# Performance work log

Measured on AMD Instinct MI355X. Metric: run time of the kernel, lower is better.

## Reference

```python
import jax, jax.numpy as jnp
import numpy as np

N_OBJ, N_REL = 2048, 32768
OBJ_DIM, POOL, H, E, C = 4096, 2048, 512, 200, 151
GEO = 128
IMG_W, IMG_H = 1024.0, 768.0
NUM_ITER = 3


def _lin(x, W, b):
    return x @ W.T + b


def _gru(x, h, Wih, Whh, bih, bhh):
    # torch.nn.GRUCell math; gates stacked (r, z, n)
    gi = x @ Wih.T + bih
    gh = h @ Whh.T + bhh
    i_r, i_z, i_n = jnp.split(gi, 3, axis=-1)
    h_r, h_z, h_n = jnp.split(gh, 3, axis=-1)
    r = jax.nn.sigmoid(i_r + h_r)
    z = jax.nn.sigmoid(i_z + h_z)
    n = jnp.tanh(i_n + r * h_n)
    return (1.0 - z) * n + z * h


def _box_info(boxes, norm=None):
    # [x1,y1,x2,y2,cx,cy,w,h]
    wh = boxes[:, 2:4] - boxes[:, 0:2] + 1.0
    ctr = boxes[:, 0:2] + 0.5 * wh
    info = jnp.concatenate([boxes, ctr, wh], axis=1)
    return info / norm if norm is not None else info


def _box_pair_info(b1, b2):
    # b1,b2: [R,8] normalized box infos -> [R,32]
    ub = jnp.stack([jnp.minimum(b1[:, 0], b2[:, 0]), jnp.minimum(b1[:, 1], b2[:, 1]),
                    jnp.maximum(b1[:, 2], b2[:, 2]), jnp.maximum(b1[:, 3], b2[:, 3])], axis=1)
    ib = jnp.stack([jnp.maximum(b1[:, 0], b2[:, 0]), jnp.maximum(b1[:, 1], b2[:, 1]),
                    jnp.minimum(b1[:, 2], b2[:, 2]), jnp.minimum(b1[:, 3], b2[:, 3])], axis=1)
    inter = _box_info(ib)
    bad = (ib[:, 2] < ib[:, 0]) | (ib[:, 3] < ib[:, 1])
    inter = jnp.where(bad[:, None], 0.0, inter)
    return jnp.concatenate([b1, b2, _box_info(ub), inter], axis=1)


def _encode_box_info(boxes):
    # motifs 9-d geometry encoding
    wh = boxes[:, 2:4] - boxes[:, 0:2] + 1.0
    xy = boxes[:, 0:2] + 0.5 * wh
    w, h = wh[:, 0:1], wh[:, 1:2]
    x, y = xy[:, 0:1], xy[:, 1:2]
    x1, y1, x2, y2 = boxes[:, 0:1], boxes[:, 1:2], boxes[:, 2:3], boxes[:, 3:4]
    return jnp.concatenate([w / IMG_W, h / IMG_H, x / IMG_W, y / IMG_H, x1 / IMG_W,
                            y1 / IMG_H, x2 / IMG_W, y2 / IMG_H, w * h / (IMG_W * IMG_H)], axis=1)


def _forward(inst_roi_feats, union_features, boxes, emb_dist_W, emb_label_W, up_W, up_b,
             pairup_W, pairup_b, pos1_W, pos1_b, bn_g, bn_b, bn_m, bn_v, pos2_W, pos2_b,
             spt1_W, spt1_b, spt2_W, spt2_b, pairfin_W, pairfin_b, objhid_W, objhid_b,
             objfin_W, objfin_b, objU_W, objU_b, edgeU_W, edgeU_b,
             egru_Wih, egru_Whh, egru_bih, egru_bhh, ngru_Wih, ngru_Whh, ngru_bih, ngru_bhh,
             svw_W, svw_b, ovw_W, ovw_b, obj_labels, sub_idx, obj_idx):
    # ---- PairwiseFeatureExtractor ----
    # pos_embed: fc(9,32) -> eval BatchNorm1d(32) -> fc(32,128) -> ReLU
    p = _lin(_encode_box_info(boxes), pos1_W, pos1_b)
    p = (p - bn_m) * bn_g / jnp.sqrt(bn_v + 1e-5) + bn_b
    pos_embed = jax.nn.relu(_lin(p, pos2_W, pos2_b))
    emb_dist = emb_dist_W[obj_labels]                       # predcls: embed GT labels
    aug = _lin(jnp.concatenate([inst_roi_feats, emb_dist, pos_embed], 1), objhid_W, objhid_b)
    augment = jnp.concatenate([emb_label_W[obj_labels], inst_roi_feats, aug], 1)  # [N,4808]
    # pairwise (edge) features: gather head/tail reps + spatial gating
    obox = _box_info(boxes, norm=max(IMG_W, IMG_H, 100.0))  # [N,8]
    fused = _lin(augment, pairup_W, pairup_b).reshape(-1, 2, H)
    pair = jnp.concatenate([fused[:, 0][sub_idx], fused[:, 1][obj_idx]], 1)  # [R,1024]
    geo = _box_pair_info(obox[sub_idx], obox[obj_idx])      # [R,32]
    spt = jax.nn.relu(_lin(jax.nn.relu(_lin(geo, spt1_W, spt1_b)), spt2_W, spt2_b))
    rel_feats = jax.nn.relu(_lin(pair * spt, pairfin_W, pairfin_b))
    rel_feats = rel_feats + _lin(union_features, up_W, up_b)  # 'fusion' + dim-up
    obj_feats = jax.nn.relu(_lin(augment, objfin_W, objfin_b))
    # ---- IMP iterative message passing ----
    obj_rep = _lin(obj_feats, objU_W, objU_b)
    rel_rep = jax.nn.relu(_lin(rel_feats, edgeU_W, edgeU_b))
    vert = _gru(obj_rep, jnp.zeros_like(obj_rep), ngru_Wih, ngru_Whh, ngru_bih, ngru_bhh)
    edge = _gru(rel_rep, jnp.zeros_like(rel_rep), egru_Wih, egru_Whh, egru_bih, egru_bhh)
    n = vert.shape[0]
    for _ in range(NUM_ITER):
        sv, ov = vert[sub_idx], vert[obj_idx]
        ws = jax.nn.sigmoid(_lin(jnp.concatenate([sv, edge], 1), svw_W, svw_b))  # [R,1]
        wo = jax.nn.sigmoid(_lin(jnp.concatenate([ov, edge], 1), ovw_W, ovw_b))
        new_edge = _gru(ws * sv + wo * ov, edge, egru_Wih, egru_Whh, egru_bih, egru_bhh)
        # sub2rel @ (ws*edge) + obj2rel @ (wo*edge) == segment sums over pair indices
        ctx = jax.ops.segment_sum(ws * edge, sub_idx, n) + jax.ops.segment_sum(wo * edge, obj_idx, n)
        vert = _gru(ctx, vert, ngru_Wih, ngru_Whh, ngru_bih, ngru_bhh)
        edge = new_edge
    return vert, edge


def setup_inputs() -> dict:
    keys = jax.random.split(jax.random.key(0), 64)
    ki = iter(keys)

    def nrm(shape, s=0.02):
        return (jax.random.normal(next(ki), shape) * s).astype(jnp.float32)

    kb = jax.random.split(next(ki), 4)
    x1 = jax.random.uniform(kb[0], (N_OBJ,)) * (IMG_W - 200.0)
    y1 = jax.random.uniform(kb[1], (N_OBJ,)) * (IMG_H - 150.0)
    x2 = x1 + 1.0 + jax.random.uniform(kb[2], (N_OBJ,)) * 199.0
    y2 = y1 + 1.0 + jax.random.uniform(kb[3], (N_OBJ,)) * 149.0
    boxes = jnp.stack([x1, y1, x2, y2], axis=1).astype(jnp.float32)

    inp = {
        'inst_roi_feats': nrm((N_OBJ, OBJ_DIM), 1.0),
        'union_features': nrm((N_REL, OBJ_DIM), 1.0),
        'boxes': boxes,
        'emb_dist_W': nrm((C, E)), 'emb_label_W': nrm((C, E)),
        'up_W': nrm((POOL, OBJ_DIM)), 'up_b': jnp.zeros((POOL,), jnp.float32),
        'pairup_W': nrm((2 * H, H + OBJ_DIM + E)), 'pairup_b': jnp.zeros((2 * H,), jnp.float32),
        'pos1_W': nrm((32, 9)), 'pos1_b': jnp.zeros((32,), jnp.float32),
        'bn_g': jnp.ones((32,), jnp.float32), 'bn_b': jnp.zeros((32,), jnp.float32),
        'bn_m': nrm((32,)), 'bn_v': jnp.ones((32,), jnp.float32),
        'pos2_W': nrm((GEO, 32)), 'pos2_b': jnp.zeros((GEO,), jnp.float32),
        'spt1_W': nrm((H, 32)), 'spt1_b': jnp.zeros((H,), jnp.float32),
        'spt2_W': nrm((2 * H, H)), 'spt2_b': jnp.zeros((2 * H,), jnp.float32),
        'pairfin_W': nrm((POOL, 2 * H)), 'pairfin_b': jnp.zeros((POOL,), jnp.float32),
        'objhid_W': nrm((H, OBJ_DIM + E + GEO)), 'objhid_b': jnp.zeros((H,), jnp.float32),
        'objfin_W': nrm((POOL, H + OBJ_DIM + E)), 'objfin_b': jnp.zeros((POOL,), jnp.float32),
        'objU_W': nrm((H, POOL)), 'objU_b': jnp.zeros((H,), jnp.float32),
        'edgeU_W': nrm((H, POOL)), 'edgeU_b': jnp.zeros((H,), jnp.float32),
        'egru_Wih': nrm((3 * H, H)), 'egru_Whh': nrm((3 * H, H)),
        'egru_bih': jnp.zeros((3 * H,), jnp.float32), 'egru_bhh': jnp.zeros((3 * H,), jnp.float32),
        'ngru_Wih': nrm((3 * H, H)), 'ngru_Whh': nrm((3 * H, H)),
        'ngru_bih': jnp.zeros((3 * H,), jnp.float32), 'ngru_bhh': jnp.zeros((3 * H,), jnp.float32),
        'svw_W': nrm((1, 2 * H)), 'svw_b': jnp.zeros((1,), jnp.float32),
        'ovw_W': nrm((1, 2 * H)), 'ovw_b': jnp.zeros((1,), jnp.float32),
        'obj_labels': jax.random.randint(next(ki), (N_OBJ,), 0, C),
        'sub_idx': jax.random.randint(next(ki), (N_REL,), 0, N_OBJ),
        'obj_idx': jax.random.randint(next(ki), (N_REL,), 0, N_OBJ),
    }
    return inp


def reference(inst_roi_feats, union_features, boxes, emb_dist_W, emb_label_W, up_W, up_b,
              pairup_W, pairup_b, pos1_W, pos1_b, bn_g, bn_b, bn_m, bn_v, pos2_W, pos2_b,
              spt1_W, spt1_b, spt2_W, spt2_b, pairfin_W, pairfin_b, objhid_W, objhid_b,
              objfin_W, objfin_b, objU_W, objU_b, edgeU_W, edgeU_b,
              egru_Wih, egru_Whh, egru_bih, egru_bhh, ngru_Wih, ngru_Whh, ngru_bih, ngru_bhh,
              svw_W, svw_b, ovw_W, ovw_b, obj_labels, sub_idx, obj_idx):
    return _forward(inst_roi_feats, union_features, boxes, emb_dist_W, emb_label_W, up_W, up_b,
                    pairup_W, pairup_b, pos1_W, pos1_b, bn_g, bn_b, bn_m, bn_v, pos2_W, pos2_b,
                    spt1_W, spt1_b, spt2_W, spt2_b, pairfin_W, pairfin_b, objhid_W, objhid_b,
                    objfin_W, objfin_b, objU_W, objU_b, edgeU_W, edgeU_b,
                    egru_Wih, egru_Whh, egru_bih, egru_bhh, ngru_Wih, ngru_Whh, ngru_bih, ngru_bhh,
                    svw_W, svw_b, ovw_W, ovw_b, obj_labels, sub_idx, obj_idx)
```

## Files before the change

### kernel.cpp

```cpp
#include <hip/hip_runtime.h>
#include <stdint.h>

#define NOBJ 2048
#define NREL 32768

typedef __attribute__((ext_vector_type(8))) short short8;
typedef __attribute__((ext_vector_type(4))) float f32x4;
typedef __attribute__((ext_vector_type(4))) unsigned short ushort4v;

__device__ __forceinline__ unsigned short f2bs(float x){
  unsigned u = __float_as_uint(x);
  unsigned v = u + 0x7fffu + ((u >> 16) & 1u);
  return (unsigned short)(v >> 16);
}
__device__ __forceinline__ float b2f(unsigned short u){
  return __uint_as_float(((unsigned)u) << 16);
}
__device__ __forceinline__ float sigf(float x){ return 1.0f / (1.0f + expf(-x)); }

__device__ __forceinline__ void gload16(const unsigned short* g, unsigned short* l) {
  __builtin_amdgcn_global_load_lds(
      (const __attribute__((address_space(1))) unsigned int*)(uintptr_t)g,
      (__attribute__((address_space(3))) unsigned int*)(uintptr_t)l,
      16, 0, 0);
}

template<int RMODE, bool ACCUM, bool OUTB, bool PRODF, bool AF32>
__global__ __launch_bounds__(256, 2)
void gemm_bt(const void* __restrict__ Ap, const unsigned short* __restrict__ B,
             const float* __restrict__ bias, const float* __restrict__ Cin,
             void* __restrict__ Cp, int M, int N, int K, int lda, int ldc,
             const unsigned short* __restrict__ fusedp,
             const int* __restrict__ subp, const int* __restrict__ objp)
{
  __shared__ __align__(16) unsigned short As[128 * 64];
  __shared__ __align__(16) unsigned short Bs[128 * 64];
  const int t = threadIdx.x;
  const int lane = t & 63;
  const int w = t >> 6;
  const int nwg = gridDim.x;
  const int q8 = nwg >> 3, r8 = nwg & 7;
  const int xcd = blockIdx.x & 7, bidx = blockIdx.x >> 3;
  const int wgid = (xcd < r8 ? xcd * (q8 + 1) : r8 * (q8 + 1) + (xcd - r8) * q8) + bidx;
  const int ntile = N >> 7;
  const int bm = wgid / ntile;
  const int bn = wgid - bm * ntile;
  const int m0 = bm << 7, n0 = bn << 7;
  const int wm = (w & 1) << 6, wn = (w >> 1) << 6;
  const int lrow = lane & 15, kg = lane >> 4;
  const int rx = lrow & 7;

  const int srow8 = lane >> 3;
  const int sslot = ((lane & 7) ^ srow8) << 3;
  const unsigned short* Bg = B + (long)(n0 + w * 8 + srow8) * K + sslot;
  const long ldb32 = (long)32 * K;

  const unsigned short* Ag = nullptr;
  const float* afp = nullptr;
  long lda32 = 0;
  int ar0 = 0;
  unsigned short* abase = nullptr;
  if constexpr (AF32) {
    ar0 = t >> 4;
    const int ac4 = t & 15;
    afp = (const float*)Ap + (long)(m0 + ar0) * lda + (ac4 << 2);
    abase = As + ((((ac4 >> 1) ^ (ar0 & 7)) << 3) + ((ac4 & 1) << 2));
  } else {
    Ag = (const unsigned short*)Ap + (long)(m0 + w * 8 + srow8) * lda + sslot;
    lda32 = (long)32 * lda;
  }

  f32x4 acc[4][4] = {};

  for (int k0 = 0; k0 < K; k0 += 64) {
#pragma unroll
    for (int q = 0; q < 4; q++)
      gload16(Bg + q * ldb32 + k0, Bs + (q * 32 + w * 8) * 64);
    if constexpr (AF32) {
      const float* ap = afp + k0;
#pragma unroll
      for (int j = 0; j < 8; j++) {
        f32x4 v = *(const f32x4*)(ap + (long)j * 16 * lda);
        ushort4v o;
        o[0] = f2bs(v[0]); o[1] = f2bs(v[1]); o[2] = f2bs(v[2]); o[3] = f2bs(v[3]);
        *(ushort4v*)(abase + (ar0 + j * 16) * 64) = o;
      }
    } else {
#pragma unroll
      for (int q = 0; q < 4; q++)
        gload16(Ag + q * lda32 + k0, As + (q * 32 + w * 8) * 64);
    }
    __syncthreads();
    short8 afr[4][2], bfr[4][2];
#pragma unroll
    for (int i = 0; i < 4; i++) {
      const int ra = wm + i * 16 + lrow;
#pragma unroll
      for (int ks = 0; ks < 2; ks++)
        afr[i][ks] = *(const short8*)(As + ra * 64 + (((ks * 4 + kg) ^ rx) << 3));
    }
#pragma unroll
    for (int j = 0; j < 4; j++) {
      const int rb = wn + j * 16 + lrow;
#pragma unroll
      for (int ks = 0; ks < 2; ks++)
        bfr[j][ks] = *(const short8*)(Bs + rb * 64 + (((ks * 4 + kg) ^ rx) << 3));
    }
#pragma unroll
    for (int i = 0; i < 4; i++)
#pragma unroll
      for (int j = 0; j < 4; j++)
#pragma unroll
        for (int ks = 0; ks < 2; ks++)
          acc[i][j] = __builtin_amdgcn_mfma_f32_16x16x32_bf16(afr[i][ks], bfr[j][ks], acc[i][j], 0, 0, 0);
    __syncthreads();
  }

  float* Cf = (float*)Cp;
  unsigned short* Cb = (unsigned short*)Cp;
#pragma unroll
  for (int i = 0; i < 4; i++) {
#pragma unroll
    for (int j = 0; j < 4; j++) {
      const int col = n0 + wn + j * 16 + lrow;
      const float bv = bias[col];
#pragma unroll
      for (int q = 0; q < 4; q++) {
        const long row = m0 + wm + i * 16 + kg * 4 + q;
        float v = acc[i][j][q] + bv;
        if constexpr (RMODE == 1) v = fmaxf(v, 0.0f);
        if constexpr (PRODF) {
          int gr = (col < 512) ? subp[row] : objp[row];
          v *= b2f(fusedp[(long)gr * 1024 + col]);
        }
        if constexpr (ACCUM) v += Cin[row * (long)N + col];
        if constexpr (RMODE == 2) v = fmaxf(v, 0.0f);
        if constexpr (OUTB) Cb[row * (long)ldc + col] = f2bs(v);
        else Cf[row * (long)ldc + col] = v;
      }
    }
  }
}

template<int RMODE>
__global__ __launch_bounds__(256, 2)
void gemm64(const unsigned short* __restrict__ A, const unsigned short* __restrict__ B,
            const float* __restrict__ bias, unsigned short* __restrict__ C,
            int M, int N, int K, int lda, int ldc)
{
  __shared__ __align__(16) unsigned short As[64 * 64];
  __shared__ __align__(16) unsigned short Bs[64 * 64];
  const int t = threadIdx.x;
  const int lane = t & 63;
  const int w = t >> 6;
  const int nwg = gridDim.x;
  const int q8 = nwg >> 3, r8 = nwg & 7;
  const int xcd = blockIdx.x & 7, bidx = blockIdx.x >> 3;
  const int wgid = (xcd < r8 ? xcd * (q8 + 1) : r8 * (q8 + 1) + (xcd - r8) * q8) + bidx;
  const int ntile = N >> 6;
  const int bm = wgid / ntile, bn = wgid - bm * ntile;
  const int m0 = bm << 6, n0 = bn << 6;
  const int wm = (w & 1) << 5, wn = (w >> 1) << 5;
  const int lrow = lane & 15, kg = lane >> 4;
  const int rx = lrow & 7;

  const int srow8 = lane >> 3;
  const int sslot = ((lane & 7) ^ srow8) << 3;
  const unsigned short* Ag = A + (long)(m0 + w * 16 + srow8) * lda + sslot;
  const unsigned short* Bg = B + (long)(n0 + w * 16 + srow8) * K + sslot;
  const long lda8 = 8L * lda, ldb8 = 8L * K;

  f32x4 acc[2][2] = {};

  for (int k0 = 0; k0 < K; k0 += 64) {
    gload16(Ag + k0,        As + (w * 16) * 64);
    gload16(Ag + lda8 + k0, As + (w * 16 + 8) * 64);
    gload16(Bg + k0,        Bs + (w * 16) * 64);
    gload16(Bg + ldb8 + k0, Bs + (w * 16 + 8) * 64);
    __syncthreads();
    short8 afr[2][2], bfr[2][2];
#pragma unroll
    for (int i = 0; i < 2; i++) {
      const int ra = wm + i * 16 + lrow;
#pragma unroll
      for (int ks = 0; ks < 2; ks++)
        afr[i][ks] = *(const short8*)(As + ra * 64 + (((ks * 4 + kg) ^ rx) << 3));
    }
#pragma unroll
    for (int j = 0; j < 2; j++) {
      const int rb = wn + j * 16 + lrow;
#pragma unroll
      for (int ks = 0; ks < 2; ks++)
        bfr[j][ks] = *(const short8*)(Bs + rb * 64 + (((ks * 4 + kg) ^ rx) << 3));
    }
#pragma unroll
    for (int i = 0; i < 2; i++)
#pragma unroll
      for (int j = 0; j < 2; j++)
#pragma unroll
        for (int ks = 0; ks < 2; ks++)
          acc[i][j] = __builtin_amdgcn_mfma_f32_16x16x32_bf16(afr[i][ks], bfr[j][ks], acc[i][j], 0, 0, 0);
    __syncthreads();
  }

#pragma unroll
  for (int i = 0; i < 2; i++) {
#pragma unroll
    for (int j = 0; j < 2; j++) {
      const int col = n0 + wn + j * 16 + lrow;
      const float bv = bias[col];
#pragma unroll
      for (int q = 0; q < 4; q++) {
        const long row = m0 + wm + i * 16 + kg * 4 + q;
        float v = acc[i][j][q] + bv;
        if constexpr (RMODE == 1) v = fmaxf(v, 0.0f);
        C[row * (long)ldc + col] = f2bs(v);
      }
    }
  }
}


__global__ void cvt_pad4(const float* __restrict__ src, unsigned short* __restrict__ dst,
                         int rows, int K0, int Kp)
{
  const int kp4 = Kp >> 2;
  const long total = (long)rows * kp4;
  for (long i = blockIdx.x * (long)blockDim.x + threadIdx.x; i < total; i += (long)gridDim.x * blockDim.x) {
    int r = (int)(i / kp4), k = (int)(i - (long)r * kp4) << 2;
    ushort4v o;
    if (k < K0) {
      f32x4 v = *(const f32x4*)(src + (long)r * K0 + k);
      o[0] = f2bs(v[0]); o[1] = f2bs(v[1]); o[2] = f2bs(v[2]); o[3] = f2bs(v[3]);
    } else {
      o[0] = 0; o[1] = 0; o[2] = 0; o[3] = 0;
    }
    *(ushort4v*)(dst + (long)r * Kp + k) = o;
  }
}

struct CvtSeg { const float* src; unsigned short* dst; long base; long n4; };
struct Cvt9 { CvtSeg s[9]; long total; };

__global__ void cvt4_multi(Cvt9 cfg)
{
  for (long i = blockIdx.x * (long)blockDim.x + threadIdx.x; i < cfg.total;
       i += (long)gridDim.x * blockDim.x) {
#pragma unroll
    for (int k = 0; k < 9; k++) {
      if (i >= cfg.s[k].base && i < cfg.s[k].base + cfg.s[k].n4) {
        long j = i - cfg.s[k].base;
        f32x4 v = ((const f32x4*)cfg.s[k].src)[j];
        ushort4v o;
        o[0] = f2bs(v[0]); o[1] = f2bs(v[1]); o[2] = f2bs(v[2]); o[3] = f2bs(v[3]);
        ((ushort4v*)cfg.s[k].dst)[j] = o;
        break;
      }
    }
  }
}

__global__ void transpose_cvt(const float* __restrict__ src, unsigned short* __restrict__ dst,
                              int R, int C)
{
  __shared__ float tile[32][33];
  int c0 = blockIdx.x * 32, r0 = blockIdx.y * 32;
  for (int i = threadIdx.y; i < 32; i += 8)
    tile[i][threadIdx.x] = src[(long)(r0 + i) * C + c0 + threadIdx.x];
  __syncthreads();
  for (int i = threadIdx.y; i < 32; i += 8)
    dst[(long)(c0 + i) * R + r0 + threadIdx.x] = f2bs(tile[threadIdx.x][i]);
}

__global__ void comp_bias(const float* __restrict__ edgeU_W, const float* __restrict__ up_b,
                          const float* __restrict__ edgeU_b, float* __restrict__ b_comp)
{
  int j = (int)((blockIdx.x * (long)blockDim.x + threadIdx.x) >> 6);
  int l = threadIdx.x & 63;
  if (j >= 512) return;
  float s = 0.0f;
  for (int k = l; k < 2048; k += 64) s += edgeU_W[(long)j * 2048 + k] * up_b[k];
#pragma unroll
  for (int off = 32; off > 0; off >>= 1) s += __shfl_xor(s, off);
  if (l == 0) b_comp[j] = s + edgeU_b[j];
}

__global__ void bias_cat(const float* __restrict__ bhh, float* __restrict__ out)
{
  int j = blockIdx.x * blockDim.x + threadIdx.x;
  if (j < 3072) out[j] = (j < 1536) ? 0.0f : bhh[j - 1536];
}

__global__ void obox_k(const float* __restrict__ boxes, float* __restrict__ obox)
{
  int i = blockIdx.x * blockDim.x + threadIdx.x;
  if (i >= NOBJ) return;
  float x1 = boxes[i*4], y1 = boxes[i*4+1], x2 = boxes[i*4+2], y2 = boxes[i*4+3];
  float wdt = x2 - x1 + 1.0f, hgt = y2 - y1 + 1.0f;
  float cx = x1 + 0.5f * wdt, cy = y1 + 0.5f * hgt;
  const float inv = 1.0f / 1024.0f;
  float* o = obox + i * 8;
  o[0]=x1*inv; o[1]=y1*inv; o[2]=x2*inv; o[3]=y2*inv;
  o[4]=cx*inv; o[5]=cy*inv; o[6]=wdt*inv; o[7]=hgt*inv;
}

__global__ void posembed_k(const float* __restrict__ boxes,
                           const float* __restrict__ w1, const float* __restrict__ b1,
                           const float* __restrict__ g, const float* __restrict__ bb,
                           const float* __restrict__ mm, const float* __restrict__ vv,
                           const float* __restrict__ w2, const float* __restrict__ b2,
                           float* __restrict__ out)
{
  int o = blockIdx.x, t = threadIdx.x;
  __shared__ float e[9];
  __shared__ float p[32];
  if (t == 0) {
    float x1 = boxes[o*4], y1 = boxes[o*4+1], x2 = boxes[o*4+2], y2 = boxes[o*4+3];
    float wdt = x2 - x1 + 1.0f, hgt = y2 - y1 + 1.0f;
    float cx = x1 + 0.5f * wdt, cy = y1 + 0.5f * hgt;
    e[0]=wdt/1024.0f; e[1]=hgt/768.0f; e[2]=cx/1024.0f; e[3]=cy/768.0f;
    e[4]=x1/1024.0f;  e[5]=y1/768.0f;  e[6]=x2/1024.0f; e[7]=y2/768.0f;
    e[8]=wdt*hgt/(1024.0f*768.0f);
  }
  __syncthreads();
  if (t < 32) {
    float s = b1[t];
#pragma unroll
    for (int j = 0; j < 9; j++) s += w1[t*9+j] * e[j];
    s = (s - mm[t]) * g[t] / sqrtf(vv[t] + 1e-5f) + bb[t];
    p[t] = s;
  }
  __syncthreads();
  float s = b2[t];
#pragma unroll
  for (int j = 0; j < 32; j++) s += w2[t*32+j] * p[j];
  out[o*128 + t] = fmaxf(s, 0.0f);
}

__device__ __forceinline__ void pack8_store(unsigned short* dst, f32x4 a, f32x4 b)
{
  ushort4v o0, o1;
  o0[0]=f2bs(a[0]); o0[1]=f2bs(a[1]); o0[2]=f2bs(a[2]); o0[3]=f2bs(a[3]);
  o1[0]=f2bs(b[0]); o1[1]=f2bs(b[1]); o1[2]=f2bs(b[2]); o1[3]=f2bs(b[3]);
  *(ushort4v*)dst = o0;
  *(ushort4v*)(dst + 4) = o1;
}

__global__ void build_x1(const float* __restrict__ inst, const float* __restrict__ embd,
                         const int* __restrict__ labels, const float* __restrict__ pose,
                         unsigned short* __restrict__ X1b)
{
  const long total = (long)NOBJ * 560;
  for (long i = blockIdx.x * (long)blockDim.x + threadIdx.x; i < total; i += (long)gridDim.x * blockDim.x) {
    int r = (int)(i / 560), c = ((int)(i - (long)r * 560)) << 3;
    unsigned short* dst = X1b + (long)r * 4480 + c;
    const float* src;
    if (c < 4096)      src = inst + (long)r * 4096 + c;
    else if (c < 4296) src = embd + (long)labels[r] * 200 + (c - 4096);
    else if (c < 4424) src = pose + r * 128 + (c - 4296);
    else { ushort4v z = {0,0,0,0}; *(ushort4v*)dst = z; *(ushort4v*)(dst+4) = z; continue; }
    pack8_store(dst, *(const f32x4*)src, *((const f32x4*)src + 1));
  }
}

__global__ void build_aug(const float* __restrict__ embl, const int* __restrict__ labels,
                          const float* __restrict__ inst, unsigned short* __restrict__ augb)
{
  const long total = (long)NOBJ * 608;
  for (long i = blockIdx.x * (long)blockDim.x + threadIdx.x; i < total; i += (long)gridDim.x * blockDim.x) {
    int r = (int)(i / 608), c = ((int)(i - (long)r * 608)) << 3;
    if (c >= 4296 && c < 4808) continue;
    unsigned short* dst = augb + (long)r * 4864 + c;
    const float* src;
    if (c < 200)       src = embl + (long)labels[r] * 200 + c;
    else if (c < 4296) src = inst + (long)r * 4096 + (c - 200);
    else { ushort4v z = {0,0,0,0}; *(ushort4v*)dst = z; *(ushort4v*)(dst+4) = z; continue; }
    pack8_store(dst, *(const f32x4*)src, *((const f32x4*)src + 1));
  }
}

__global__ void build_geo(const float* __restrict__ obox, const int* __restrict__ sub,
                          const int* __restrict__ obj, unsigned short* __restrict__ geob)
{
  int r = blockIdx.x * blockDim.x + threadIdx.x;
  if (r >= NREL) return;
  const float* b1 = obox + sub[r] * 8;
  const float* b2 = obox + obj[r] * 8;
  float o[32];
#pragma unroll
  for (int j = 0; j < 8; j++) { o[j] = b1[j]; o[8+j] = b2[j]; }
  float ux1 = fminf(b1[0], b2[0]), uy1 = fminf(b1[1], b2[1]);
  float ux2 = fmaxf(b1[2], b2[2]), uy2 = fmaxf(b1[3], b2[3]);
  float uw = ux2 - ux1 + 1.0f, uh = uy2 - uy1 + 1.0f;
  o[16]=ux1; o[17]=uy1; o[18]=ux2; o[19]=uy2;
  o[20]=ux1+0.5f*uw; o[21]=uy1+0.5f*uh; o[22]=uw; o[23]=uh;
  float ix1 = fmaxf(b1[0], b2[0]), iy1 = fmaxf(b1[1], b2[1]);
  float ix2 = fminf(b1[2], b2[2]), iy2 = fminf(b1[3], b2[3]);
  bool bad = (ix2 < ix1) || (iy2 < iy1);
  float iw = ix2 - ix1 + 1.0f, ih = iy2 - iy1 + 1.0f;
  if (bad) {
#pragma unroll
    for (int j = 24; j < 32; j++) o[j] = 0.0f;
  } else {
    o[24]=ix1; o[25]=iy1; o[26]=ix2; o[27]=iy2;
    o[28]=ix1+0.5f*iw; o[29]=iy1+0.5f*ih; o[30]=iw; o[31]=ih;
  }
  unsigned short* gp = geob + (long)r * 64;
#pragma unroll
  for (int j = 0; j < 32; j++) gp[j] = f2bs(o[j]);
#pragma unroll
  for (int j = 32; j < 64; j++) gp[j] = 0;
}

__global__ void gru_init_v(const unsigned short* __restrict__ gi, const float* __restrict__ bhh,
                           float* __restrict__ h, unsigned short* __restrict__ hb, int n)
{
  const long total = (long)n * 64;
  for (long i = blockIdx.x * (long)blockDim.x + threadIdx.x; i < total; i += (long)gridDim.x * blockDim.x) {
    int r = (int)(i >> 6), c = ((int)(i & 63)) << 3;
    const unsigned short* gr = gi + (long)r * 1536;
    short8 vr = *(const short8*)(gr + c);
    short8 vz = *(const short8*)(gr + 512 + c);
    short8 vn = *(const short8*)(gr + 1024 + c);
    float hv[8];
#pragma unroll
    for (int k = 0; k < 8; k++) {
      float rr = sigf(b2f((unsigned short)vr[k]) + bhh[c + k]);
      float z  = sigf(b2f((unsigned short)vz[k]) + bhh[512 + c + k]);
      float nn = tanhf(b2f((unsigned short)vn[k]) + rr * bhh[1024 + c + k]);
      hv[k] = (1.0f - z) * nn;
    }
    float* hp = h + (long)r * 512 + c;
    *(f32x4*)hp = *(f32x4*)hv;
    *(f32x4*)(hp + 4) = *(f32x4*)(hv + 4);
    pack8_store(hb + (long)r * 512 + c, *(f32x4*)hv, *(f32x4*)(hv + 4));
  }
}

__global__ void gru_init_e(const unsigned short* __restrict__ gi, const float* __restrict__ bhh,
                           unsigned short* __restrict__ hb, int n)
{
  const long total = (long)n * 64;
  for (long i = blockIdx.x * (long)blockDim.x + threadIdx.x; i < total; i += (long)gridDim.x * blockDim.x) {
    int r = (int)(i >> 6), c = ((int)(i & 63)) << 3;
    const unsigned short* gr = gi + (long)r * 1536;
    short8 vr = *(const short8*)(gr + c);
    short8 vz = *(const short8*)(gr + 512 + c);
    short8 vn = *(const short8*)(gr + 1024 + c);
    float hv[8];
#pragma unroll
    for (int k = 0; k < 8; k++) {
      float rr = sigf(b2f((unsigned short)vr[k]) + bhh[c + k]);
      float z  = sigf(b2f((unsigned short)vz[k]) + bhh[512 + c + k]);
      float nn = tanhf(b2f((unsigned short)vn[k]) + rr * bhh[1024 + c + k]);
      hv[k] = (1.0f - z) * nn;
    }
    pack8_store(hb + (long)r * 512 + c, *(f32x4*)hv, *(f32x4*)(hv + 4));
  }
}

__global__ void gru_step_v(const unsigned short* __restrict__ gi, const unsigned short* __restrict__ gh,
                           int ghs, const float* __restrict__ hin, float* __restrict__ hout,
                           unsigned short* __restrict__ hb, int n)
{
  const long total = (long)n * 64;
  for (long i = blockIdx.x * (long)blockDim.x + threadIdx.x; i < total; i += (long)gridDim.x * blockDim.x) {
    int r = (int)(i >> 6), c = ((int)(i & 63)) << 3;
    const unsigned short* gr = gi + (long)r * 1536;
    const unsigned short* hr = gh + (long)r * ghs;
    short8 ir = *(const short8*)(gr + c);
    short8 iz = *(const short8*)(gr + 512 + c);
    short8 in_ = *(const short8*)(gr + 1024 + c);
    short8 hrr = *(const short8*)(hr + c);
    short8 hz = *(const short8*)(hr + 512 + c);
    short8 hn = *(const short8*)(hr + 1024 + c);
    const float* hi = hin + (long)r * 512 + c;
    f32x4 h0 = *(const f32x4*)hi;
    f32x4 h1 = *(const f32x4*)(hi + 4);
    float hv[8];
#pragma unroll
    for (int k = 0; k < 8; k++) {
      float rr = sigf(b2f((unsigned short)ir[k]) + b2f((unsigned short)hrr[k]));
      float z  = sigf(b2f((unsigned short)iz[k]) + b2f((unsigned short)hz[k]));
      float nn = tanhf(b2f((unsigned short)in_[k]) + rr * b2f((unsigned short)hn[k]));
      float old = (k < 4) ? h0[k] : h1[k - 4];
      hv[k] = (1.0f - z) * nn + z * old;
    }
    float* hp = hout + (long)r * 512 + c;
    *(f32x4*)hp = *(f32x4*)hv;
    *(f32x4*)(hp + 4) = *(f32x4*)(hv + 4);
    pack8_store(hb + (long)r * 512 + c, *(f32x4*)hv, *(f32x4*)(hv + 4));
  }
}

__global__ __launch_bounds__(256)
void gru_step_e2(const unsigned short* __restrict__ GH, const unsigned short* __restrict__ VG,
                 const float* __restrict__ ws_arr_in, const float* __restrict__ wo_arr_in,
                 float* __restrict__ ws_arr_out, float* __restrict__ wo_arr_out,
                 const int* __restrict__ sub, const int* __restrict__ obj,
                 const float* __restrict__ bih,
                 unsigned short* __restrict__ edgeb, float* __restrict__ fout,
                 const unsigned short* __restrict__ vertb,
                 const float* __restrict__ svwW, const float* __restrict__ svwb,
                 const float* __restrict__ ovwW, const float* __restrict__ ovwb,
                 int compute_w, int n)
{
  long gid = blockIdx.x * 256L + threadIdx.x;
  int r = (int)(gid >> 6);
  int l = (int)(gid & 63);
  if (r >= n) return;
  const int c = l << 3;
  int s = sub[r], o = obj[r];
  float ws = ws_arr_in[r], wo = wo_arr_in[r];
  const unsigned short* gh = GH + (long)r * 1536;
  const unsigned short* vs = VG + (long)s * 3072;
  const unsigned short* vo = VG + (long)o * 3072;
  short8 ghr = *(const short8*)(gh + c);
  short8 ghz = *(const short8*)(gh + 512 + c);
  short8 ghn = *(const short8*)(gh + 1024 + c);
  short8 vsr = *(const short8*)(vs + c);
  short8 vsz = *(const short8*)(vs + 512 + c);
  short8 vsn = *(const short8*)(vs + 1024 + c);
  short8 vor_ = *(const short8*)(vo + c);
  short8 voz = *(const short8*)(vo + 512 + c);
  short8 von = *(const short8*)(vo + 1024 + c);
  short8 hold = *(const short8*)(edgeb + (long)r * 512 + c);
  float hv[8];
#pragma unroll
  for (int k = 0; k < 8; k++) {
    float gir = ws * b2f((unsigned short)vsr[k]) + wo * b2f((unsigned short)vor_[k]) + bih[c + k];
    float giz = ws * b2f((unsigned short)vsz[k]) + wo * b2f((unsigned short)voz[k]) + bih[512 + c + k];
    float gin = ws * b2f((unsigned short)vsn[k]) + wo * b2f((unsigned short)von[k]) + bih[1024 + c + k];
    float rr = sigf(gir + b2f((unsigned short)ghr[k]));
    float z  = sigf(giz + b2f((unsigned short)ghz[k]));
    float nn = tanhf(gin + rr * b2f((unsigned short)ghn[k]));
    hv[k] = (1.0f - z) * nn + z * b2f((unsigned short)hold[k]);
  }
  pack8_store(edgeb + (long)r * 512 + c, *(f32x4*)hv, *(f32x4*)(hv + 4));
  if (fout) {
    float* fp = fout + (long)r * 512 + c;
    *(f32x4*)fp = *(f32x4*)hv;
    *(f32x4*)(fp + 4) = *(f32x4*)(hv + 4);
  }
  if (compute_w) {
    short8 svv = *(const short8*)(vertb + (long)s * 512 + c);
    short8 ovv = *(const short8*)(vertb + (long)o * 512 + c);
    float as = 0.0f, ao = 0.0f;
#pragma unroll
    for (int k = 0; k < 8; k++) {
      float e = hv[k];
      as += svwW[c + k] * b2f((unsigned short)svv[k]) + svwW[512 + c + k] * e;
      ao += ovwW[c + k] * b2f((unsigned short)ovv[k]) + ovwW[512 + c + k] * e;
    }
#pragma unroll
    for (int off = 32; off > 0; off >>= 1) {
      as += __shfl_xor(as, off);
      ao += __shfl_xor(ao, off);
    }
    if (l == 0) {
      ws_arr_out[r] = sigf(as + svwb[0]);
      wo_arr_out[r] = sigf(ao + ovwb[0]);
    }
  }
}

__global__ __launch_bounds__(256)
void edge_weights(const unsigned short* __restrict__ vertb, const unsigned short* __restrict__ edgeb,
                  const int* __restrict__ sub, const int* __restrict__ obj,
                  const float* __restrict__ svwW, const float* __restrict__ svwb,
                  const float* __restrict__ ovwW, const float* __restrict__ ovwb,
                  float* __restrict__ ws_arr, float* __restrict__ wo_arr)
{
  long gid = blockIdx.x * 256L + threadIdx.x;
  int r = (int)(gid >> 6);
  int l = (int)(gid & 63);
  if (r >= NREL) return;
  int s = sub[r], o = obj[r];
  const unsigned short* sv = vertb + (long)s * 512;
  const unsigned short* ov = vertb + (long)o * 512;
  const unsigned short* e  = edgeb + (long)r * 512;
  float as = 0.0f, ao = 0.0f;
#pragma unroll
  for (int k = 0; k < 8; k++) {
    int c = l + k * 64;
    float svv = b2f(sv[c]), ovv = b2f(ov[c]), ev = b2f(e[c]);
    as += svwW[c] * svv + svwW[512 + c] * ev;
    ao += ovwW[c] * ovv + ovwW[512 + c] * ev;
  }
#pragma unroll
  for (int off = 32; off > 0; off >>= 1) {
    as += __shfl_xor(as, off);
    ao += __shfl_xor(ao, off);
  }
  if (l == 0) {
    ws_arr[r] = sigf(as + svwb[0]);
    wo_arr[r] = sigf(ao + ovwb[0]);
  }
}


__global__ void csr_count(const int* __restrict__ sub, const int* __restrict__ obj,
                          int* __restrict__ cnt)
{
  int r = blockIdx.x * blockDim.x + threadIdx.x;
  if (r >= NREL) return;
  atomicAdd(&cnt[sub[r]], 1);
  atomicAdd(&cnt[obj[r]], 1);
}

__global__ __launch_bounds__(1024)
void csr_scan(const int* __restrict__ cnt, int* __restrict__ off)
{
  __shared__ int a[1024], b[1024];
  int t = threadIdx.x;
  int c0 = cnt[2*t], c1 = cnt[2*t+1];
  a[t] = c0 + c1;
  __syncthreads();
  int* src = a; int* dst = b;
  for (int s = 1; s < 1024; s <<= 1) {
    int v = src[t];
    if (t >= s) v += src[t - s];
    dst[t] = v;
    __syncthreads();
    int* tmp = src; src = dst; dst = tmp;
  }
  int incl = src[t];
  int excl = incl - (c0 + c1);
  off[2*t] = excl;
  off[2*t+1] = excl + c0;
  if (t == 1023) off[2048] = incl;
}

__global__ void csr_fill(const int* __restrict__ sub, const int* __restrict__ obj,
                         const int* __restrict__ off, int* __restrict__ rcur,
                         int* __restrict__ lists)
{
  int r = blockIdx.x * blockDim.x + threadIdx.x;
  if (r >= NREL) return;
  int s = sub[r];
  int p = atomicAdd(&rcur[s], 1);
  lists[off[s] + p] = (r << 1);
  int o = obj[r];
  int q = atomicAdd(&rcur[o], 1);
  lists[off[o] + q] = (r << 1) | 1;
}

__global__ __launch_bounds__(128)
void ctx_gather(const unsigned short* __restrict__ edgeb, const float* __restrict__ ws,
                const float* __restrict__ wo, const int* __restrict__ off,
                const int* __restrict__ lists, unsigned short* __restrict__ ctxb)
{
  __shared__ float part[512];
  int o = blockIdx.x;
  int l = threadIdx.x & 63;
  int w = threadIdx.x >> 6;
  int i0 = off[o], i1 = off[o + 1];
  float acc[8] = {0.f,0.f,0.f,0.f,0.f,0.f,0.f,0.f};
  for (int i = i0 + w; i < i1; i += 2) {
    int e = lists[i];
    int r = e >> 1;
    float sc = (e & 1) ? wo[r] : ws[r];
    short8 row = *(const short8*)(edgeb + (long)r * 512 + l * 8);
#pragma unroll
    for (int k = 0; k < 8; k++) acc[k] += sc * b2f((unsigned short)row[k]);
  }
  if (w == 1) {
    *(f32x4*)&part[l*8]     = *(f32x4*)&acc[0];
    *(f32x4*)&part[l*8 + 4] = *(f32x4*)&acc[4];
  }
  __syncthreads();
  if (w == 0) {
#pragma unroll
    for (int k = 0; k < 8; k++) acc[k] += part[l*8 + k];
    pack8_store(ctxb + (long)o * 512 + l * 8, *(f32x4*)&acc[0], *(f32x4*)&acc[4]);
  }
}


static inline int nblk(long total) {
  long b = (total + 255) / 256;
  return (int)(b > 16384 ? 16384 : b);
}

#define GEMM(RM, AC, OB, PF, grid, Aa, Bb, bb, Ci, Cc, Mm, Nn, Kk, ldA, ldC, fp, sp, op) \
  gemm_bt<RM, AC, OB, PF, false><<<grid, 256, 0, stream>>>(Aa, Bb, bb, Ci, Cc, Mm, Nn, Kk, ldA, ldC, fp, sp, op)
#define GEMMF(RM, AC, OB, grid, Aa, Bb, bb, Ci, Cc, Mm, Nn, Kk, ldA, ldC) \
  gemm_bt<RM, AC, OB, false, true><<<grid, 256, 0, stream>>>(Aa, Bb, bb, Ci, Cc, Mm, Nn, Kk, ldA, ldC, nullptr, nullptr, nullptr)
#define G64(RM, Aa, Bb, bb, Cc, Mm, Nn, Kk, ldA, ldC) \
  gemm64<RM><<<dim3(((Mm) >> 6) * ((Nn) >> 6)), 256, 0, stream>>>(Aa, Bb, bb, Cc, Mm, Nn, Kk, ldA, ldC)

extern "C" void kernel_launch(void* const* d_in, const int* in_sizes, int n_in,
                              void* d_out, int out_size, void* d_ws, size_t ws_size,
                              hipStream_t stream)
{
  const float* inst     = (const float*)d_in[0];
  const float* unionf   = (const float*)d_in[1];
  const float* boxes    = (const float*)d_in[2];
  const float* embd_W   = (const float*)d_in[3];
  const float* embl_W   = (const float*)d_in[4];
  const float* up_W     = (const float*)d_in[5];
  const float* up_b     = (const float*)d_in[6];
  const float* pairup_W = (const float*)d_in[7];
  const float* pairup_b = (const float*)d_in[8];
  const float* pos1_W   = (const float*)d_in[9];
  const float* pos1_b   = (const float*)d_in[10];
  const float* bn_g     = (const float*)d_in[11];
  const float* bn_b     = (const float*)d_in[12];
  const float* bn_m     = (const float*)d_in[13];
  const float* bn_v     = (const float*)d_in[14];
  const float* pos2_W   = (const float*)d_in[15];
  const float* pos2_b   = (const float*)d_in[16];
  const float* spt1_W   = (const float*)d_in[17];
  const float* spt1_b   = (const float*)d_in[18];
  const float* spt2_W   = (const float*)d_in[19];
  const float* spt2_b   = (const float*)d_in[20];
  const float* pairfin_W= (const float*)d_in[21];
  const float* pairfin_b= (const float*)d_in[22];
  const float* objhid_W = (const float*)d_in[23];
  const float* objhid_b = (const float*)d_in[24];
  const float* objfin_W = (const float*)d_in[25];
  const float* objfin_b = (const float*)d_in[26];
  const float* objU_W   = (const float*)d_in[27];
  const float* objU_b   = (const float*)d_in[28];
  const float* edgeU_W  = (const float*)d_in[29];
  const float* edgeU_b  = (const float*)d_in[30];
  const float* egru_Wih = (const float*)d_in[31];
  const float* egru_Whh = (const float*)d_in[32];
  const float* egru_bih = (const float*)d_in[33];
  const float* egru_bhh = (const float*)d_in[34];
  const float* ngru_Wih = (const float*)d_in[35];
  const float* ngru_Whh = (const float*)d_in[36];
  const float* ngru_bih = (const float*)d_in[37];
  const float* ngru_bhh = (const float*)d_in[38];
  const float* svw_W    = (const float*)d_in[39];
  const float* svw_b    = (const float*)d_in[40];
  const float* ovw_W    = (const float*)d_in[41];
  const float* ovw_b    = (const float*)d_in[42];
  const int*   labels   = (const int*)d_in[43];
  const int*   sub      = (const int*)d_in[44];
  const int*   obj      = (const int*)d_in[45];
  (void)in_sizes; (void)n_in; (void)out_size; (void)ws_size;

  char* base = (char*)d_ws;
  size_t off = 0;
  auto alloc = [&](size_t bytes) -> void* {
    void* p = base + off;
    off += (bytes + 255) & ~(size_t)255;
    return p;
  };

  unsigned short* objhid_Wb  = (unsigned short*)alloc(512L  * 4480 * 2);
  unsigned short* pairup_Wb  = (unsigned short*)alloc(1024L * 4864 * 2);
  unsigned short* objfin_Wb  = (unsigned short*)alloc(2048L * 4864 * 2);
  unsigned short* up_Wtb     = (unsigned short*)alloc(4096L * 2048 * 2);
  unsigned short* pairfin_Wb = (unsigned short*)alloc(2048L * 1024 * 2);
  unsigned short* spt1_Wb    = (unsigned short*)alloc(512L  * 64   * 2);
  unsigned short* spt2_Wb    = (unsigned short*)alloc(1024L * 512  * 2);
  unsigned short* objU_Wb    = (unsigned short*)alloc(512L  * 2048 * 2);
  unsigned short* edgeU_Wb   = (unsigned short*)alloc(512L  * 2048 * 2);
  unsigned short* egru_Wihb  = (unsigned short*)alloc(1536L * 512  * 2);
  unsigned short* egru_Whhb  = (unsigned short*)alloc(1536L * 512  * 2);
  unsigned short* ngru_Wihb  = (unsigned short*)alloc(1536L * 512  * 2);
  unsigned short* vg_Wb      = (unsigned short*)alloc(3072L * 512  * 2);
  unsigned short* W_compb    = (unsigned short*)alloc(512L  * 4096 * 2);
  float*          b_comp     = (float*)alloc(512L * 4);
  float*          zbias      = (float*)alloc(4096L * 4);
  float*          vgbias     = (float*)alloc(3072L * 4);

  float*          obox      = (float*)alloc(NOBJ * 8L * 4);
  float*          pose      = (float*)alloc(NOBJ * 128L * 4);
  unsigned short* obj_featsb= (unsigned short*)alloc((long)NOBJ * 2048 * 2);
  unsigned short* obj_repb  = (unsigned short*)alloc((long)NOBJ * 512 * 2);
  unsigned short* giv       = (unsigned short*)alloc((long)NOBJ * 1536 * 2);
  unsigned short* VGb       = (unsigned short*)alloc((long)NOBJ * 3072 * 2);
  float*          vert      = (float*)alloc((long)NOBJ * 512 * 4);
  unsigned short* vertb     = (unsigned short*)alloc((long)NOBJ * 512 * 2);
  unsigned short* ctxb      = (unsigned short*)alloc((long)NOBJ * 512 * 2);
  unsigned short* geob      = (unsigned short*)alloc((long)NREL * 64 * 2);
  unsigned short* edgeb     = (unsigned short*)alloc((long)NREL * 512 * 2);
  float*          ws_arr    = (float*)alloc((long)NREL * 4);
  float*          wo_arr    = (float*)alloc((long)NREL * 4);

  int* cnt   = (int*)alloc(NOBJ * 4);
  int* coff  = (int*)alloc((NOBJ + 1) * 4);
  int* rcur  = (int*)alloc(NOBJ * 4);
  int* lists = (int*)alloc(2L * NREL * 4);

  char* regA = (char*)alloc((long)NREL * 512 * 4);
  unsigned short* X1b = (unsigned short*)regA;
  float*          T1  = (float*)regA;
  char* regB = (char*)alloc((long)NOBJ * 4864 * 2 > (long)NREL * 512 * 2
                            ? (long)NOBJ * 4864 * 2 : (long)NREL * 512 * 2);
  unsigned short* augb     = (unsigned short*)regB;
  unsigned short* rel_repb = (unsigned short*)regB;
  unsigned short* fusedb = (unsigned short*)alloc((long)NOBJ * 1024 * 2);
  unsigned short* spt1b  = (unsigned short*)alloc((long)NREL * 512 * 2);
  char* big1 = (char*)alloc((long)NREL * 1536 * 4);
  unsigned short* G1    = (unsigned short*)big1;
  unsigned short* prodb = (unsigned short*)(big1 + (long)NREL * 1024 * 4);
  unsigned short* gi_e  = (unsigned short*)big1;
  unsigned short* GHb   = (unsigned short*)big1;

  float* d_out_vert = (float*)d_out;
  float* d_out_edge = (float*)d_out + (long)NOBJ * 512;

  cvt_pad4<<<nblk(512L*4480/4),  256, 0, stream>>>(objhid_W,  objhid_Wb,  512,  4424, 4480);
  cvt_pad4<<<nblk(1024L*4864/4), 256, 0, stream>>>(pairup_W,  pairup_Wb,  1024, 4808, 4864);
  cvt_pad4<<<nblk(2048L*4864/4), 256, 0, stream>>>(objfin_W,  objfin_Wb,  2048, 4808, 4864);
  cvt_pad4<<<nblk(512L*64/4),    256, 0, stream>>>(spt1_W,    spt1_Wb,    512,  32,   64);
  {
    Cvt9 cfg;
    long b = 0;
    auto seg = [&](int k, const float* s, unsigned short* d, long n4) {
      cfg.s[k].src = s; cfg.s[k].dst = d; cfg.s[k].base = b; cfg.s[k].n4 = n4; b += n4;
    };
    seg(0, pairfin_W, pairfin_Wb, 2048L*1024/4);
    seg(1, spt2_W,    spt2_Wb,    1024L*512/4);
    seg(2, objU_W,    objU_Wb,    512L*2048/4);
    seg(3, edgeU_W,   edgeU_Wb,   512L*2048/4);
    seg(4, egru_Wih,  egru_Wihb,  1536L*512/4);
    seg(5, egru_Whh,  egru_Whhb,  1536L*512/4);
    seg(6, ngru_Wih,  ngru_Wihb,  1536L*512/4);
    seg(7, egru_Wih,  vg_Wb,              1536L*512/4);
    seg(8, ngru_Whh,  vg_Wb + 1536L*512,  1536L*512/4);
    cfg.total = b;
    cvt4_multi<<<nblk(b), 256, 0, stream>>>(cfg);
  }
  bias_cat<<<12, 256, 0, stream>>>(ngru_bhh, vgbias);
  transpose_cvt<<<dim3(4096/32, 2048/32), dim3(32, 8), 0, stream>>>(up_W, up_Wtb, 2048, 4096);
  hipMemsetAsync(zbias, 0, 4096L * 4, stream);
  comp_bias<<<128, 256, 0, stream>>>(edgeU_W, up_b, edgeU_b, b_comp);
  G64(0, edgeU_Wb, up_Wtb, zbias, W_compb, 512, 4096, 2048, 2048, 4096);

  hipMemsetAsync(cnt, 0, NOBJ * 4, stream);
  hipMemsetAsync(rcur, 0, NOBJ * 4, stream);
  csr_count<<<NREL/256, 256, 0, stream>>>(sub, obj, cnt);
  csr_scan<<<1, 1024, 0, stream>>>(cnt, coff);
  csr_fill<<<NREL/256, 256, 0, stream>>>(sub, obj, coff, rcur, lists);

  obox_k<<<(NOBJ + 255) / 256, 256, 0, stream>>>(boxes, obox);
  posembed_k<<<NOBJ, 128, 0, stream>>>(boxes, pos1_W, pos1_b, bn_g, bn_b, bn_m, bn_v,
                                       pos2_W, pos2_b, pose);
  build_x1<<<nblk((long)NOBJ*560), 256, 0, stream>>>(inst, embd_W, labels, pose, X1b);
  build_aug<<<nblk((long)NOBJ*608), 256, 0, stream>>>(embl_W, labels, inst, augb);
  G64(0, X1b, objhid_Wb, objhid_b, augb + 4296, NOBJ, 512, 4480, 4480, 4864);
  G64(0, augb, pairup_Wb, pairup_b, fusedb, NOBJ, 1024, 4864, 4864, 1024);
  G64(1, augb, objfin_Wb, objfin_b, obj_featsb, NOBJ, 2048, 4864, 4864, 2048);
  G64(0, obj_featsb, objU_Wb, objU_b, obj_repb, NOBJ, 512, 2048, 2048, 512);
  G64(0, obj_repb, ngru_Wihb, ngru_bih, giv, NOBJ, 1536, 512, 512, 1536);
  gru_init_v<<<nblk((long)NOBJ*64), 256, 0, stream>>>(giv, ngru_bhh, vert, vertb, NOBJ);

  build_geo<<<(NREL + 255) / 256, 256, 0, stream>>>(obox, sub, obj, geob);
  GEMM(1,false,true ,false, dim3((NREL>>7)*(512>>7)),  geob, spt1_Wb, spt1_b, nullptr, spt1b, NREL, 512, 64, 64, 512, nullptr, nullptr, nullptr);
  GEMM(1,false,true ,true , dim3((NREL>>7)*(1024>>7)), spt1b, spt2_Wb, spt2_b, nullptr, prodb, NREL, 1024, 512, 512, 1024, fusedb, sub, obj);
  GEMM(1,false,true ,false, dim3((NREL>>7)*(2048>>7)), prodb, pairfin_Wb, pairfin_b, nullptr, G1, NREL, 2048, 1024, 1024, 2048, nullptr, nullptr, nullptr);
  GEMMF(0,false,false, dim3((NREL>>7)*(512>>7)), unionf, W_compb, b_comp, nullptr, T1, NREL, 512, 4096, 4096, 512);
  GEMM(2,true ,true ,false, dim3((NREL>>7)*(512>>7)),  G1, edgeU_Wb, zbias, T1, rel_repb, NREL, 512, 2048, 2048, 512, nullptr, nullptr, nullptr);
  GEMM(0,false,true ,false, dim3((NREL>>7)*(1536>>7)), rel_repb, egru_Wihb, egru_bih, nullptr, gi_e, NREL, 1536, 512, 512, 1536, nullptr, nullptr, nullptr);
  gru_init_e<<<nblk((long)NREL*64), 256, 0, stream>>>(gi_e, egru_bhh, edgeb, NREL);

  edge_weights<<<NREL*64/256, 256, 0, stream>>>(vertb, edgeb, sub, obj,
                                                svw_W, svw_b, ovw_W, ovw_b, ws_arr, wo_arr);

  for (int it = 0; it < 3; it++) {
    const bool last = (it == 2);
    ctx_gather<<<NOBJ, 128, 0, stream>>>(edgeb, ws_arr, wo_arr, coff, lists, ctxb);
    G64(0, vertb, vg_Wb, vgbias, VGb, NOBJ, 3072, 512, 512, 3072);
    GEMM(0,false,true,false, dim3((NREL>>7)*(1536>>7)), edgeb, egru_Whhb, egru_bhh, nullptr, GHb, NREL, 1536, 512, 512, 1536, nullptr, nullptr, nullptr);
    G64(0, ctxb, ngru_Wihb, ngru_bih, giv, NOBJ, 1536, 512, 512, 1536);
    gru_step_v<<<nblk((long)NOBJ*64), 256, 0, stream>>>(giv, VGb + 1536, 3072, vert,
                                                        last ? d_out_vert : vert, vertb, NOBJ);
    gru_step_e2<<<NREL*64/256, 256, 0, stream>>>(GHb, VGb, ws_arr, wo_arr, ws_arr, wo_arr,
                                                 sub, obj, egru_bih, edgeb,
                                                 last ? d_out_edge : nullptr, vertb,
                                                 svw_W, svw_b, ovw_W, ovw_b,
                                                 last ? 0 : 1, NREL);
  }
}
```

Baseline: 1.695 ms.

## Double-buffer LDS tiles in GEMM kernels and store intermediate T1 as bf16

Both GEMM kernels now use two LDS buffers and prefetch the tiles two k-steps ahead, with explicit vmcnt waits and raw barriers, so global loads overlap with MFMA work. gemm64 raises its launch_bounds occupancy hint from 2 to 4. The union-feature GEMM intermediate T1 is now written as bf16 and read back as bf16 in the accumulating GEMM, which halves that traffic at some precision cost. Doubling LDS in gemm_bt to 64KB may reduce occupancy, and the hand-written waitcnt counts must match the number of issued loads exactly.

```diff
diff --git a/kernel.cpp b/kernel.cpp
--- a/kernel.cpp
+++ b/kernel.cpp
@@ -25,16 +25,16 @@
       16, 0, 0);
 }
 
-template<int RMODE, bool ACCUM, bool OUTB, bool PRODF, bool AF32>
+template<int RMODE, bool ACCUM, bool OUTB, bool PRODF, bool AF32, bool CINB>
 __global__ __launch_bounds__(256, 2)
 void gemm_bt(const void* __restrict__ Ap, const unsigned short* __restrict__ B,
-             const float* __restrict__ bias, const float* __restrict__ Cin,
+             const float* __restrict__ bias, const void* __restrict__ Cin,
              void* __restrict__ Cp, int M, int N, int K, int lda, int ldc,
              const unsigned short* __restrict__ fusedp,
              const int* __restrict__ subp, const int* __restrict__ objp)
 {
-  __shared__ __align__(16) unsigned short As[128 * 64];
-  __shared__ __align__(16) unsigned short Bs[128 * 64];
+  __shared__ __align__(16) unsigned short As[2][128 * 64];
+  __shared__ __align__(16) unsigned short Bs[2][128 * 64];
   const int t = threadIdx.x;
   const int lane = t & 63;
   const int w = t >> 6;
@@ -58,53 +58,74 @@
   const unsigned short* Ag = nullptr;
   const float* afp = nullptr;
   long lda32 = 0;
-  int ar0 = 0;
-  unsigned short* abase = nullptr;
+  int ar0 = 0, aoff = 0;
   if constexpr (AF32) {
     ar0 = t >> 4;
     const int ac4 = t & 15;
     afp = (const float*)Ap + (long)(m0 + ar0) * lda + (ac4 << 2);
-    abase = As + ((((ac4 >> 1) ^ (ar0 & 7)) << 3) + ((ac4 & 1) << 2));
+    aoff = (((ac4 >> 1) ^ (ar0 & 7)) << 3) + ((ac4 & 1) << 2);
   } else {
     Ag = (const unsigned short*)Ap + (long)(m0 + w * 8 + srow8) * lda + sslot;
     lda32 = (long)32 * lda;
   }
 
-  f32x4 acc[4][4] = {};
-
-  for (int k0 = 0; k0 < K; k0 += 64) {
+  const int NT = K >> 6;
+
+  auto stage = [&](int buf, int kt) {
+    const unsigned short* bsrc = Bg + (long)kt * 64;
 #pragma unroll
     for (int q = 0; q < 4; q++)
-      gload16(Bg + q * ldb32 + k0, Bs + (q * 32 + w * 8) * 64);
+      gload16(bsrc + q * ldb32, Bs[buf] + (q * 32 + w * 8) * 64);
     if constexpr (AF32) {
-      const float* ap = afp + k0;
+      const float* ap = afp + (long)kt * 64;
 #pragma unroll
       for (int j = 0; j < 8; j++) {
         f32x4 v = *(const f32x4*)(ap + (long)j * 16 * lda);
         ushort4v o;
         o[0] = f2bs(v[0]); o[1] = f2bs(v[1]); o[2] = f2bs(v[2]); o[3] = f2bs(v[3]);
-        *(ushort4v*)(abase + (ar0 + j * 16) * 64) = o;
+        *(ushort4v*)(As[buf] + aoff + (ar0 + j * 16) * 64) = o;
       }
     } else {
+      const unsigned short* asrc = Ag + (long)kt * 64;
 #pragma unroll
       for (int q = 0; q < 4; q++)
-        gload16(Ag + q * lda32 + k0, As + (q * 32 + w * 8) * 64);
-    }
-    __syncthreads();
+        gload16(asrc + q * lda32, As[buf] + (q * 32 + w * 8) * 64);
+    }
+  };
+
+  f32x4 acc[4][4] = {};
+
+  stage(0, 0);
+  if (NT > 1) stage(1, 1);
+
+  for (int kt = 0; kt < NT; ++kt) {
+    const int cur = kt & 1;
+    if (kt + 1 < NT) {
+      if constexpr (AF32) asm volatile("s_waitcnt vmcnt(4)" ::: "memory");
+      else                asm volatile("s_waitcnt vmcnt(8)" ::: "memory");
+    } else {
+      asm volatile("s_waitcnt vmcnt(0)" ::: "memory");
+    }
+    asm volatile("s_waitcnt lgkmcnt(0)" ::: "memory");
+    __builtin_amdgcn_s_barrier();
+    asm volatile("" ::: "memory");
+
+    const unsigned short* As_ = As[cur];
+    const unsigned short* Bs_ = Bs[cur];
     short8 afr[4][2], bfr[4][2];
 #pragma unroll
     for (int i = 0; i < 4; i++) {
       const int ra = wm + i * 16 + lrow;
 #pragma unroll
       for (int ks = 0; ks < 2; ks++)
-        afr[i][ks] = *(const short8*)(As + ra * 64 + (((ks * 4 + kg) ^ rx) << 3));
+        afr[i][ks] = *(const short8*)(As_ + ra * 64 + (((ks * 4 + kg) ^ rx) << 3));
     }
 #pragma unroll
     for (int j = 0; j < 4; j++) {
       const int rb = wn + j * 16 + lrow;
 #pragma unroll
       for (int ks = 0; ks < 2; ks++)
-        bfr[j][ks] = *(const short8*)(Bs + rb * 64 + (((ks * 4 + kg) ^ rx) << 3));
+        bfr[j][ks] = *(const short8*)(Bs_ + rb * 64 + (((ks * 4 + kg) ^ rx) << 3));
     }
 #pragma unroll
     for (int i = 0; i < 4; i++)
@@ -113,7 +134,10 @@
 #pragma unroll
         for (int ks = 0; ks < 2; ks++)
           acc[i][j] = __builtin_amdgcn_mfma_f32_16x16x32_bf16(afr[i][ks], bfr[j][ks], acc[i][j], 0, 0, 0);
-    __syncthreads();
+    asm volatile("" ::: "memory");
+    __builtin_amdgcn_s_barrier();
+    asm volatile("" ::: "memory");
+    if (kt + 2 < NT) stage(cur, kt + 2);
   }
 
   float* Cf = (float*)Cp;
@@ -133,7 +157,10 @@
           int gr = (col < 512) ? subp[row] : objp[row];
           v *= b2f(fusedp[(long)gr * 1024 + col]);
         }
-        if constexpr (ACCUM) v += Cin[row * (long)N + col];
+        if constexpr (ACCUM) {
+          if constexpr (CINB) v += b2f(((const unsigned short*)Cin)[row * (long)N + col]);
+          else                v += ((const float*)Cin)[row * (long)N + col];
+        }
         if constexpr (RMODE == 2) v = fmaxf(v, 0.0f);
         if constexpr (OUTB) Cb[row * (long)ldc + col] = f2bs(v);
         else Cf[row * (long)ldc + col] = v;
@@ -143,13 +170,13 @@
 }
 
 template<int RMODE>
-__global__ __launch_bounds__(256, 2)
+__global__ __launch_bounds__(256, 4)
 void gemm64(const unsigned short* __restrict__ A, const unsigned short* __restrict__ B,
             const float* __restrict__ bias, unsigned short* __restrict__ C,
             int M, int N, int K, int lda, int ldc)
 {
-  __shared__ __align__(16) unsigned short As[64 * 64];
-  __shared__ __align__(16) unsigned short Bs[64 * 64];
+  __shared__ __align__(16) unsigned short As[2][64 * 64];
+  __shared__ __align__(16) unsigned short Bs[2][64 * 64];
   const int t = threadIdx.x;
   const int lane = t & 63;
   const int w = t >> 6;
@@ -169,29 +196,45 @@
   const unsigned short* Ag = A + (long)(m0 + w * 16 + srow8) * lda + sslot;
   const unsigned short* Bg = B + (long)(n0 + w * 16 + srow8) * K + sslot;
   const long lda8 = 8L * lda, ldb8 = 8L * K;
+  const int NT = K >> 6;
+
+  auto stage = [&](int buf, int kt) {
+    const unsigned short* a_ = Ag + (long)kt * 64;
+    const unsigned short* b_ = Bg + (long)kt * 64;
+    gload16(a_,        As[buf] + (w * 16) * 64);
+    gload16(a_ + lda8, As[buf] + (w * 16 + 8) * 64);
+    gload16(b_,        Bs[buf] + (w * 16) * 64);
+    gload16(b_ + ldb8, Bs[buf] + (w * 16 + 8) * 64);
+  };
 
   f32x4 acc[2][2] = {};
 
-  for (int k0 = 0; k0 < K; k0 += 64) {
-    gload16(Ag + k0,        As + (w * 16) * 64);
-    gload16(Ag + lda8 + k0, As + (w * 16 + 8) * 64);
-    gload16(Bg + k0,        Bs + (w * 16) * 64);
-    gload16(Bg + ldb8 + k0, Bs + (w * 16 + 8) * 64);
-    __syncthreads();
+  stage(0, 0);
+  if (NT > 1) stage(1, 1);
+
+  for (int kt = 0; kt < NT; ++kt) {
+    const int cur = kt & 1;
+    if (kt + 1 < NT) asm volatile("s_waitcnt vmcnt(4)" ::: "memory");
+    else             asm volatile("s_waitcnt vmcnt(0)" ::: "memory");
+    __builtin_amdgcn_s_barrier();
+    asm volatile("" ::: "memory");
+
+    const unsigned short* As_ = As[cur];
+    const unsigned short* Bs_ = Bs[cur];
     short8 afr[2][2], bfr[2][2];
 #pragma unroll
     for (int i = 0; i < 2; i++) {
       const int ra = wm + i * 16 + lrow;
 #pragma unroll
       for (int ks = 0; ks < 2; ks++)
-        afr[i][ks] = *(const short8*)(As + ra * 64 + (((ks * 4 + kg) ^ rx) << 3));
+        afr[i][ks] = *(const short8*)(As_ + ra * 64 + (((ks * 4 + kg) ^ rx) << 3));
     }
 #pragma unroll
     for (int j = 0; j < 2; j++) {
       const int rb = wn + j * 16 + lrow;
 #pragma unroll
       for (int ks = 0; ks < 2; ks++)
-        bfr[j][ks] = *(const short8*)(Bs + rb * 64 + (((ks * 4 + kg) ^ rx) << 3));
+        bfr[j][ks] = *(const short8*)(Bs_ + rb * 64 + (((ks * 4 + kg) ^ rx) << 3));
     }
 #pragma unroll
     for (int i = 0; i < 2; i++)
@@ -200,7 +243,10 @@
 #pragma unroll
         for (int ks = 0; ks < 2; ks++)
           acc[i][j] = __builtin_amdgcn_mfma_f32_16x16x32_bf16(afr[i][ks], bfr[j][ks], acc[i][j], 0, 0, 0);
-    __syncthreads();
+    asm volatile("" ::: "memory");
+    __builtin_amdgcn_s_barrier();
+    asm volatile("" ::: "memory");
+    if (kt + 2 < NT) stage(cur, kt + 2);
   }
 
 #pragma unroll
@@ -683,9 +729,11 @@
 }
 
 #define GEMM(RM, AC, OB, PF, grid, Aa, Bb, bb, Ci, Cc, Mm, Nn, Kk, ldA, ldC, fp, sp, op) \
-  gemm_bt<RM, AC, OB, PF, false><<<grid, 256, 0, stream>>>(Aa, Bb, bb, Ci, Cc, Mm, Nn, Kk, ldA, ldC, fp, sp, op)
-#define GEMMF(RM, AC, OB, grid, Aa, Bb, bb, Ci, Cc, Mm, Nn, Kk, ldA, ldC) \
-  gemm_bt<RM, AC, OB, false, true><<<grid, 256, 0, stream>>>(Aa, Bb, bb, Ci, Cc, Mm, Nn, Kk, ldA, ldC, nullptr, nullptr, nullptr)
+  gemm_bt<RM, AC, OB, PF, false, false><<<grid, 256, 0, stream>>>(Aa, Bb, bb, Ci, Cc, Mm, Nn, Kk, ldA, ldC, fp, sp, op)
+#define GEMMCB(RM, grid, Aa, Bb, bb, Ci, Cc, Mm, Nn, Kk, ldA, ldC) \
+  gemm_bt<RM, true, true, false, false, true><<<grid, 256, 0, stream>>>(Aa, Bb, bb, Ci, Cc, Mm, Nn, Kk, ldA, ldC, nullptr, nullptr, nullptr)
+#define GEMMF(RM, grid, Aa, Bb, bb, Cc, Mm, Nn, Kk, ldA, ldC) \
+  gemm_bt<RM, false, true, false, true, false><<<grid, 256, 0, stream>>>(Aa, Bb, bb, nullptr, Cc, Mm, Nn, Kk, ldA, ldC, nullptr, nullptr, nullptr)
 #define G64(RM, Aa, Bb, bb, Cc, Mm, Nn, Kk, ldA, ldC) \
   gemm64<RM><<<dim3(((Mm) >> 6) * ((Nn) >> 6)), 256, 0, stream>>>(Aa, Bb, bb, Cc, Mm, Nn, Kk, ldA, ldC)
 
@@ -788,7 +836,7 @@
 
   char* regA = (char*)alloc((long)NREL * 512 * 4);
   unsigned short* X1b = (unsigned short*)regA;
-  float*          T1  = (float*)regA;
+  unsigned short* T1b = (unsigned short*)regA;
   char* regB = (char*)alloc((long)NOBJ * 4864 * 2 > (long)NREL * 512 * 2
                             ? (long)NOBJ * 4864 * 2 : (long)NREL * 512 * 2);
   unsigned short* augb     = (unsigned short*)regB;
@@ -854,8 +902,8 @@
   GEMM(1,false,true ,false, dim3((NREL>>7)*(512>>7)),  geob, spt1_Wb, spt1_b, nullptr, spt1b, NREL, 512, 64, 64, 512, nullptr, nullptr, nullptr);
   GEMM(1,false,true ,true , dim3((NREL>>7)*(1024>>7)), spt1b, spt2_Wb, spt2_b, nullptr, prodb, NREL, 1024, 512, 512, 1024, fusedb, sub, obj);
   GEMM(1,false,true ,false, dim3((NREL>>7)*(2048>>7)), prodb, pairfin_Wb, pairfin_b, nullptr, G1, NREL, 2048, 1024, 1024, 2048, nullptr, nullptr, nullptr);
-  GEMMF(0,false,false, dim3((NREL>>7)*(512>>7)), unionf, W_compb, b_comp, nullptr, T1, NREL, 512, 4096, 4096, 512);
-  GEMM(2,true ,true ,false, dim3((NREL>>7)*(512>>7)),  G1, edgeU_Wb, zbias, T1, rel_repb, NREL, 512, 2048, 2048, 512, nullptr, nullptr, nullptr);
+  GEMMF(0, dim3((NREL>>7)*(512>>7)), unionf, W_compb, b_comp, T1b, NREL, 512, 4096, 4096, 512);
+  GEMMCB(2, dim3((NREL>>7)*(512>>7)), G1, edgeU_Wb, zbias, T1b, rel_repb, NREL, 512, 2048, 2048, 512);
   GEMM(0,false,true ,false, dim3((NREL>>7)*(1536>>7)), rel_repb, egru_Wihb, egru_bih, nullptr, gi_e, NREL, 1536, 512, 512, 1536, nullptr, nullptr, nullptr);
   gru_init_e<<<nblk((long)NREL*64), 256, 0, stream>>>(gi_e, egru_bhh, edgeb, NREL);
 
```

After: 1.672 ms. No clear change (-1.4%).
